# Kernel tuning notes

Measured on AMD Instinct MI355X. Metric: run time of the kernel, lower is better.

Reference implementation:

```python
import jax, jax.numpy as jnp
import numpy as np

F_DIM = 512
N_HEADS = 8
D_Q = 64
D_V = 64
EPS = 1e-6


def _xavier(key, shape):
    fan_in, fan_out = shape[0], shape[1]
    limit = float(np.sqrt(6.0 / (fan_in + fan_out)))
    return jax.random.uniform(key, shape, jnp.float32, -limit, limit)


def layer_norm(x, g, b):
    mu = jnp.mean(x, axis=-1, keepdims=True)
    var = jnp.mean(jnp.square(x - mu), axis=-1, keepdims=True)
    return (x - mu) * jax.lax.rsqrt(var + EPS) * g + b


def setup_inputs() -> dict:
    key = jax.random.key(0)
    ks = jax.random.split(key, 16)
    B, V, F = 4, 2048, F_DIM
    inp = {
        "texture_map1": jax.random.normal(ks[0], (B, V, F), jnp.float32),
        "texture_map2": jax.random.normal(ks[1], (B, V, F), jnp.float32),
        "ln1_g": jnp.ones((F,), jnp.float32), "ln1_b": jnp.zeros((F,), jnp.float32),
        "ln2_g": jnp.ones((F,), jnp.float32), "ln2_b": jnp.zeros((F,), jnp.float32),
        "Wq": _xavier(ks[2], (F, N_HEADS * D_Q)), "bq": jnp.zeros((N_HEADS * D_Q,), jnp.float32),
        "Wk": _xavier(ks[3], (F, N_HEADS * D_Q)), "bk": jnp.zeros((N_HEADS * D_Q,), jnp.float32),
        "Wv": _xavier(ks[4], (F, N_HEADS * D_V)), "bv": jnp.zeros((N_HEADS * D_V,), jnp.float32),
        "Wfc": _xavier(ks[5], (N_HEADS * D_V, F)), "bfc": jnp.zeros((F,), jnp.float32),
        "ff1_ln_g": jnp.ones((F,), jnp.float32), "ff1_ln_b": jnp.zeros((F,), jnp.float32),
        "ff1_W1": _xavier(ks[6], (F, F)), "ff1_b1": jnp.zeros((F,), jnp.float32),
        "ff1_W2": _xavier(ks[7], (F, F)), "ff1_b2": jnp.zeros((F,), jnp.float32),
        "ff2_ln_g": jnp.ones((F,), jnp.float32), "ff2_ln_b": jnp.zeros((F,), jnp.float32),
        "ff2_W1": _xavier(ks[8], (F, F)), "ff2_b1": jnp.zeros((F,), jnp.float32),
        "ff2_W2": _xavier(ks[9], (F, F)), "ff2_b2": jnp.zeros((F,), jnp.float32),
    }
    return inp


def _heads(x, d):
    B, V, _ = x.shape
    return x.reshape(B, V, N_HEADS, d).transpose(0, 2, 1, 3)  # [B,H,V,d]


def _ff_block(x, ln_g, ln_b, W1, b1, W2, b2):
    h = layer_norm(x, ln_g, ln_b)
    h = jax.nn.relu(h @ W1 + b1) @ W2 + b2
    return x + h


def reference(texture_map1, texture_map2, ln1_g, ln1_b, ln2_g, ln2_b,
              Wq, bq, Wk, bk, Wv, bv, Wfc, bfc,
              ff1_ln_g, ff1_ln_b, ff1_W1, ff1_b1, ff1_W2, ff1_b2,
              ff2_ln_g, ff2_ln_b, ff2_W1, ff2_b1, ff2_W2, ff2_b2):
    B, V, F = texture_map1.shape
    norm = D_Q ** 0.5
    t1n = layer_norm(texture_map1, ln1_g, ln1_b)
    t2n = layer_norm(texture_map2, ln2_g, ln2_b)
    q1 = _heads(t1n @ Wq + bq, D_Q)
    k1 = _heads(t1n @ Wk + bk, D_Q)
    v1 = _heads(t1n @ Wv + bv, D_V)
    q2 = _heads(t2n @ Wq + bq, D_Q)
    k2 = _heads(t2n @ Wk + bk, D_Q)
    v2 = _heads(t2n @ Wv + bv, D_V)
    # cross attention: 1 attends to 2, 2 attends to 1
    attn12 = jax.nn.softmax(jnp.einsum('bhqd,bhkd->bhqk', q1, k2) / norm, axis=-1)
    attn21 = jax.nn.softmax(jnp.einsum('bhqd,bhkd->bhqk', q2, k1) / norm, axis=-1)
    f12 = jnp.einsum('bhqk,bhkd->bhqd', attn12, v2).transpose(0, 2, 1, 3).reshape(B, V, -1)
    f21 = jnp.einsum('bhqk,bhkd->bhqd', attn21, v1).transpose(0, 2, 1, 3).reshape(B, V, -1)
    f12 = f12 @ Wfc + bfc
    f21 = f21 @ Wfc + bfc
    out1 = _ff_block(texture_map1 + f12, ff1_ln_g, ff1_ln_b, ff1_W1, ff1_b1, ff1_W2, ff1_b2)
    out2 = _ff_block(texture_map2 + f21, ff2_ln_g, ff2_ln_b, ff2_W1, ff2_b1, ff2_W2, ff2_b2)
    return (out1, out2)
```

## Files before the change

### kernel.cpp

```cpp
#include <hip/hip_runtime.h>
#include <stdint.h>

#define FD    512
#define SEQ   2048
#define NHALF 8192
#define NTOT  16384
#define QKVN  1536

typedef unsigned short u16;
typedef __attribute__((ext_vector_type(8))) short short8;
typedef __attribute__((ext_vector_type(4))) float f32x4;

__device__ __forceinline__ u16 f2bf(float f){
  union { float f; uint32_t i; } v; v.f = f;
  uint32_t r = v.i + 0x7FFFu + ((v.i >> 16) & 1u);
  return (u16)(r >> 16);
}

__device__ __forceinline__ void gload_lds16(const void* g, void* l){
  __builtin_amdgcn_global_load_lds((const __attribute__((address_space(1))) void*)g,
                                   (__attribute__((address_space(3))) void*)l, 16, 0, 0);
}

__device__ __forceinline__ f32x4 mfma16(short8 a, short8 b, f32x4 c){
  return __builtin_amdgcn_mfma_f32_16x16x32_bf16(a, b, c, 0, 0, 0);
}

__device__ __forceinline__ uint32_t cvtpk(float lo, float hi){
  uint32_t r; asm("v_cvt_pk_bf16_f32 %0, %1, %2" : "=v"(r) : "v"(lo), "v"(hi)); return r;
}

__device__ __forceinline__ float fexp2(float x){
  float r; asm("v_exp_f32 %0, %1" : "=v"(r) : "v"(x)); return r;
}

__global__ __launch_bounds__(256) void wconv_kernel(
    const float* __restrict__ w0, const float* __restrict__ w1,
    const float* __restrict__ w2, const float* __restrict__ w3,
    const float* __restrict__ w4, const float* __restrict__ w5,
    const float* __restrict__ w6, const float* __restrict__ w7,
    u16* __restrict__ out)
{
  int mat = blockIdx.x >> 6;
  const float* w = w0;
  switch (mat){ case 1: w=w1; break; case 2: w=w2; break; case 3: w=w3; break;
                case 4: w=w4; break; case 5: w=w5; break; case 6: w=w6; break;
                case 7: w=w7; break; default: break; }
  int tile = blockIdx.x & 63;
  int k0 = (tile >> 3) << 6, n0 = (tile & 7) << 6;

  __shared__ float lt[64][65];
  int tid = threadIdx.x;
  int tr = tid >> 4, tc = (tid & 15) << 2;
  #pragma unroll
  for (int p = 0; p < 4; p++){
    int k = p * 16 + tr;
    float4 v = *(const float4*)&w[(size_t)(k0 + k) * 512 + n0 + tc];
    lt[k][tc] = v.x; lt[k][tc + 1] = v.y; lt[k][tc + 2] = v.z; lt[k][tc + 3] = v.w;
  }
  __syncthreads();
  int n = tid >> 2, kc = (tid & 3) << 4;
  u16 buf[16];
  #pragma unroll
  for (int j = 0; j < 16; j++) buf[j] = f2bf(lt[kc + j][n]);
  u16* dst = out + ((size_t)mat << 18) + (size_t)(n0 + n) * 512 + k0 + kc;
  *(short8*)dst       = *(const short8*)(buf);
  *(short8*)(dst + 8) = *(const short8*)(buf + 8);
}

__global__ __launch_bounds__(256) void biascat_kernel(
    const float* __restrict__ bq, const float* __restrict__ bk,
    const float* __restrict__ bv, float* __restrict__ o)
{
  int i = blockIdx.x * 256 + threadIdx.x;
  if (i < 512) o[i] = bq[i];
  else if (i < 1024) o[i] = bk[i - 512];
  else o[i] = bv[i - 1024];
}

__global__ __launch_bounds__(256) void ln_kernel(
    const float* __restrict__ xa, const float* __restrict__ xb,
    const float* __restrict__ ga, const float* __restrict__ ba,
    const float* __restrict__ gb, const float* __restrict__ bb,
    u16* __restrict__ out)
{
  int row = blockIdx.x;
  const float* x; const float* g; const float* bi;
  if (row < NHALF){ x = xa + (size_t)row * FD; g = ga; bi = ba; }
  else            { x = xb + (size_t)(row - NHALF) * FD; g = gb; bi = bb; }
  int t = threadIdx.x;
  float2 v = ((const float2*)x)[t];
  __shared__ float red[8];
  float s = v.x + v.y;
  #pragma unroll
  for (int o = 32; o; o >>= 1) s += __shfl_xor(s, o, 64);
  if ((t & 63) == 0) red[t >> 6] = s;
  __syncthreads();
  float mu = (red[0] + red[1] + red[2] + red[3]) * (1.0f / 512.0f);
  float d0 = v.x - mu, d1 = v.y - mu;
  float q = d0 * d0 + d1 * d1;
  #pragma unroll
  for (int o = 32; o; o >>= 1) q += __shfl_xor(q, o, 64);
  if ((t & 63) == 0) red[4 + (t >> 6)] = q;
  __syncthreads();
  float var = (red[4] + red[5] + red[6] + red[7]) * (1.0f / 512.0f);
  float rs = rsqrtf(var + 1e-6f);
  out[(size_t)row * FD + 2 * t]     = f2bf(d0 * rs * g[2 * t]     + bi[2 * t]);
  out[(size_t)row * FD + 2 * t + 1] = f2bf(d1 * rs * g[2 * t + 1] + bi[2 * t + 1]);
}

__global__ __launch_bounds__(256) void vtr_kernel(
    const u16* __restrict__ qkv, u16* __restrict__ vt)
{
  int kc = blockIdx.x & 15;
  int s  = blockIdx.x >> 4;
  int dir = s >> 5, b = (s >> 3) & 3, h = s & 7;
  int t = threadIdx.x;
  int d = t & 63, kb = t >> 6;
  const u16* src = qkv + (size_t)(dir * NHALF + b * SEQ + kc * 128 + kb * 32) * QKVN
                       + 1024 + h * 64 + d;
  u16* dst = vt + (size_t)s * 131072 + (size_t)d * 2048 + kc * 128 + kb * 32;
  u16 buf[32];
  #pragma unroll
  for (int j = 0; j < 32; j++) buf[j] = src[(size_t)j * QKVN];
  #pragma unroll
  for (int j = 0; j < 4; j++)
    *(short8*)(dst + j * 8) = *(const short8*)(buf + j * 8);
}

template<bool RELU, bool OUT_BF16, bool HAS_RES>
__global__ __launch_bounds__(256) void gemm_bt(
    const u16* __restrict__ A,
    const u16* __restrict__ BtLo, const u16* __restrict__ BtHi,
    const float* __restrict__ biasLo, const float* __restrict__ biasHi,
    const float* __restrict__ resLo, const float* __restrict__ resHi,
    void* __restrict__ outp,
    int M, int N, int K, int halfM)
{
  __shared__ __align__(16) u16 lA[2][128 * 32];
  __shared__ __align__(16) u16 lB[2][128 * 32];
  int nTN = N >> 7;
  int bm = blockIdx.x / nTN, bn = blockIdx.x - bm * nTN;
  int rowBase = bm << 7, colBase = bn << 7;
  bool lo = rowBase < halfM;
  const u16* Bt = lo ? BtLo : BtHi;
  const float* bias = lo ? biasLo : biasHi;
  const float* res = lo ? resLo : resHi;
  int rowLocalBase = lo ? rowBase : rowBase - halfM;

  int tid = threadIdx.x, wv = tid >> 6, ln = tid & 63;

  f32x4 acc[4][4];
  #pragma unroll
  for (int m = 0; m < 4; m++)
    #pragma unroll
    for (int n = 0; n < 4; n++) acc[m][n] = (f32x4){0.f, 0.f, 0.f, 0.f};

  int off0 = tid * 16, off1 = 4096 + tid * 16;
  int r0 = off0 >> 6, c0 = (off0 & 63) >> 1;
  int r1 = off1 >> 6, c1 = (off1 & 63) >> 1;
  const u16* gA0 = A + (size_t)(rowBase + r0) * K + c0;
  const u16* gA1 = A + (size_t)(rowBase + r1) * K + c1;
  const u16* gB0 = Bt + (size_t)(colBase + r0) * K + c0;
  const u16* gB1 = Bt + (size_t)(colBase + r1) * K + c1;

  int arow = (wv >> 1) << 6, bcol = (wv & 1) << 6;

  #define STAGE(buf, kt) do { \
    gload_lds16(gA0 + (kt), (char*)lA[buf] + wv * 1024); \
    gload_lds16(gA1 + (kt), (char*)lA[buf] + 4096 + wv * 1024); \
    gload_lds16(gB0 + (kt), (char*)lB[buf] + wv * 1024); \
    gload_lds16(gB1 + (kt), (char*)lB[buf] + 4096 + wv * 1024); } while (0)

  STAGE(0, 0);
  __syncthreads();

  int nK = K >> 5;
  for (int i = 0; i < nK; i++){
    int cur = i & 1;
    if (i + 1 < nK) STAGE(cur ^ 1, (i + 1) << 5);
    short8 af[4], bfr[4];
    #pragma unroll
    for (int m = 0; m < 4; m++)
      af[m] = *(const short8*)&lA[cur][(arow + (m << 4) + (ln & 15)) * 32 + ((ln >> 4) << 3)];
    #pragma unroll
    for (int n = 0; n < 4; n++)
      bfr[n] = *(const short8*)&lB[cur][(bcol + (n << 4) + (ln & 15)) * 32 + ((ln >> 4) << 3)];
    #pragma unroll
    for (int m = 0; m < 4; m++)
      #pragma unroll
      for (int n = 0; n < 4; n++)
        acc[m][n] = mfma16(af[m], bfr[n], acc[m][n]);
    __syncthreads();
  }
  #undef STAGE

  #pragma unroll
  for (int n = 0; n < 4; n++){
    int col = colBase + bcol + (n << 4) + (ln & 15);
    float bv = bias[col];
    #pragma unroll
    for (int m = 0; m < 4; m++){
      int rowT = arow + (m << 4) + ((ln >> 4) << 2);
      #pragma unroll
      for (int r = 0; r < 4; r++){
        float v = acc[m][n][r] + bv;
        if (RELU) v = fmaxf(v, 0.f);
        if (HAS_RES) v += res[(size_t)(rowLocalBase + rowT + r) * N + col];
        if (OUT_BF16) ((u16*)outp)[(size_t)(rowBase + rowT + r) * N + col] = f2bf(v);
        else ((float*)outp)[(size_t)(rowBase + rowT + r) * N + col] = v;
      }
    }
  }
}

__global__ __launch_bounds__(512, 4) void attn_kernel(
    const u16* __restrict__ qkv, const u16* __restrict__ vt, u16* __restrict__ fb)
{
  int qt = blockIdx.x;
  int h  = blockIdx.y;
  int z  = blockIdx.z;
  int dir = z >> 2, b = z & 3;
  int qRow0  = dir * NHALF + b * SEQ + qt * 256;
  int kvRow0 = (dir ^ 1) * NHALF + b * SEQ;
  int colQ = h * 64;

  __shared__ __align__(16) u16 lK[2][64 * 64];
  __shared__ __align__(16) u16 lVt[2][64 * 64];
  __shared__ __align__(16) u16 lP[8][32 * 64];

  int tid = threadIdx.x, wv = tid >> 6, ln = tid & 63;
  int g = ln >> 4, lo = ln & 15;

  int srow = tid >> 3;
  int soff = ((tid & 7) ^ (srow & 7)) * 8;

  const float CEXP = 0.18033688f;

  int ca0 = (g * 8) ^ ((lo & 7) << 3);
  int ca1 = (32 + g * 8) ^ ((lo & 7) << 3);
  int lo64 = lo * 64;

  int pidx[4];
  #pragma unroll
  for (int n = 0; n < 4; n++)
    pidx[n] = lo64 + ((n * 16 + g * 4) ^ ((lo & 7) << 3));
  int pra = lo64 + ca0, prb = lo64 + ca1;

  const u16* qbase  = qkv + (size_t)qRow0 * QKVN + colQ;
  const u16* vtbase = vt + (size_t)((dir ^ 1) * 32 + b * 8 + h) * 131072;

  const u16* kp0 = qkv + (size_t)(kvRow0 + srow) * QKVN + 512 + colQ + soff;
  const u16* vp0 = vtbase + (size_t)srow * 2048 + soff;

  char* dK0 = (char*)lK[0] + wv * 1024;
  char* dV0 = (char*)lVt[0] + wv * 1024;
  const u16* lKf = &lK[0][0];
  const u16* lVf = &lVt[0][0];
  u16* lPw = &lP[wv][0];

  gload_lds16(qbase + (size_t)srow * QKVN + soff,         (char*)lK[0]  + wv * 1024);
  gload_lds16(qbase + (size_t)(64 + srow) * QKVN + soff,  (char*)lK[1]  + wv * 1024);
  gload_lds16(qbase + (size_t)(128 + srow) * QKVN + soff, (char*)lVt[0] + wv * 1024);
  gload_lds16(qbase + (size_t)(192 + srow) * QKVN + soff, (char*)lVt[1] + wv * 1024);
  __syncthreads();
  const u16* qh;
  switch (wv >> 1){ case 0: qh = lK[0]; break; case 1: qh = lK[1]; break;
                    case 2: qh = lVt[0]; break; default: qh = lVt[1]; break; }
  int qr0 = (wv & 1) * 32 + lo;
  short8 qf00 = *(const short8*)&qh[qr0 * 64 + ca0];
  short8 qf01 = *(const short8*)&qh[qr0 * 64 + ca1];
  short8 qf10 = *(const short8*)&qh[(qr0 + 16) * 64 + ca0];
  short8 qf11 = *(const short8*)&qh[(qr0 + 16) * 64 + ca1];
  __syncthreads();

  gload_lds16(kp0, dK0);
  gload_lds16(vp0, dV0);
  kp0 += (size_t)64 * QKVN; vp0 += 64;
  __syncthreads();

  f32x4 acc_o0[4], acc_o1[4];
  #pragma unroll
  for (int nd = 0; nd < 4; nd++){
    acc_o0[nd] = (f32x4){0.f, 0.f, 0.f, 0.f};
    acc_o1[nd] = (f32x4){0.f, 0.f, 0.f, 0.f};
  }
  f32x4 acc_l0 = (f32x4){0.f, 0.f, 0.f, 0.f};
  f32x4 acc_l1 = (f32x4){0.f, 0.f, 0.f, 0.f};
  float m_l0, m_l1;
  const f32x4 z4 = (f32x4){0.f, 0.f, 0.f, 0.f};

  short8 ones;
  #pragma unroll
  for (int j = 0; j < 8; j++) ones[j] = (short)0x3F80;

  int cb = 0;
  for (int t = 0; t < 32; t++){
    if (t < 31){
      int nb = cb ^ 8192;
      gload_lds16(kp0, dK0 + nb);
      gload_lds16(vp0, dV0 + nb);
      kp0 += (size_t)64 * QKVN; vp0 += 64;
    }
    const u16* lk = (const u16*)((const char*)lKf + cb);
    const u16* lv = (const u16*)((const char*)lVf + cb);

    f32x4 s0[4], s1[4];
    #pragma unroll
    for (int n = 0; n < 4; n++){
      short8 kfa = *(const short8*)&lk[lo64 + n * 1024 + ca0];
      short8 kfb = *(const short8*)&lk[lo64 + n * 1024 + ca1];
      s0[n] = mfma16(kfa, qf00, z4);
      s0[n] = mfma16(kfb, qf01, s0[n]);
      s1[n] = mfma16(kfa, qf10, z4);
      s1[n] = mfma16(kfb, qf11, s1[n]);
    }

    float m00, m01;
    {
      float t0 = fmaxf(fmaxf(s0[0][0], s0[0][1]), fmaxf(s0[0][2], s0[0][3]));
      float t1 = fmaxf(fmaxf(s0[1][0], s0[1][1]), fmaxf(s0[1][2], s0[1][3]));
      float t2 = fmaxf(fmaxf(s0[2][0], s0[2][1]), fmaxf(s0[2][2], s0[2][3]));
      float t3 = fmaxf(fmaxf(s0[3][0], s0[3][1]), fmaxf(s0[3][2], s0[3][3]));
      m00 = fmaxf(fmaxf(t0, t1), fmaxf(t2, t3));
      m00 = fmaxf(m00, __shfl_xor(m00, 16, 64));
      m00 = fmaxf(m00, __shfl_xor(m00, 32, 64));
      m00 *= CEXP;
    }
    {
      float t0 = fmaxf(fmaxf(s1[0][0], s1[0][1]), fmaxf(s1[0][2], s1[0][3]));
      float t1 = fmaxf(fmaxf(s1[1][0], s1[1][1]), fmaxf(s1[1][2], s1[1][3]));
      float t2 = fmaxf(fmaxf(s1[2][0], s1[2][1]), fmaxf(s1[2][2], s1[2][3]));
      float t3 = fmaxf(fmaxf(s1[3][0], s1[3][1]), fmaxf(s1[3][2], s1[3][3]));
      m01 = fmaxf(fmaxf(t0, t1), fmaxf(t2, t3));
      m01 = fmaxf(m01, __shfl_xor(m01, 16, 64));
      m01 = fmaxf(m01, __shfl_xor(m01, 32, 64));
      m01 *= CEXP;
    }

    if (t == 0){ m_l0 = m00; m_l1 = m01; }

    #pragma unroll
    for (int n = 0; n < 4; n++){
      float p0 = fexp2(fmaf(s0[n][0], CEXP, -m_l0));
      float p1 = fexp2(fmaf(s0[n][1], CEXP, -m_l0));
      float p2 = fexp2(fmaf(s0[n][2], CEXP, -m_l0));
      float p3 = fexp2(fmaf(s0[n][3], CEXP, -m_l0));
      uint2 pk0; pk0.x = cvtpk(p0, p1); pk0.y = cvtpk(p2, p3);
      *(uint2*)&lPw[pidx[n]] = pk0;
      float q0 = fexp2(fmaf(s1[n][0], CEXP, -m_l1));
      float q1 = fexp2(fmaf(s1[n][1], CEXP, -m_l1));
      float q2 = fexp2(fmaf(s1[n][2], CEXP, -m_l1));
      float q3 = fexp2(fmaf(s1[n][3], CEXP, -m_l1));
      uint2 pk1; pk1.x = cvtpk(q0, q1); pk1.y = cvtpk(q2, q3);
      *(uint2*)&lPw[pidx[n] + 1024] = pk1;
    }

    short8 pf00 = *(const short8*)&lPw[pra];
    short8 pf01 = *(const short8*)&lPw[prb];
    short8 pf10 = *(const short8*)&lPw[pra + 1024];
    short8 pf11 = *(const short8*)&lPw[prb + 1024];
    acc_l0 = mfma16(pf00, ones, acc_l0);
    acc_l0 = mfma16(pf01, ones, acc_l0);
    acc_l1 = mfma16(pf10, ones, acc_l1);
    acc_l1 = mfma16(pf11, ones, acc_l1);
    #pragma unroll
    for (int nd = 0; nd < 4; nd++){
      short8 vfa = *(const short8*)&lv[lo64 + nd * 1024 + ca0];
      short8 vfb = *(const short8*)&lv[lo64 + nd * 1024 + ca1];
      acc_o0[nd] = mfma16(pf00, vfa, acc_o0[nd]);
      acc_o0[nd] = mfma16(pf01, vfb, acc_o0[nd]);
      acc_o1[nd] = mfma16(pf10, vfa, acc_o1[nd]);
      acc_o1[nd] = mfma16(pf11, vfb, acc_o1[nd]);
    }

    bool ok = (m00 <= m_l0 + 8.f) && (m01 <= m_l1 + 8.f);
    if (!__all(ok)){
      float mn0 = fmaxf(m_l0, m00);
      float mn1 = fmaxf(m_l1, m01);
      float a00 = fexp2(m_l0 - mn0);
      float a01 = fexp2(m_l1 - mn1);
      m_l0 = mn0; m_l1 = mn1;
      #pragma unroll
      for (int r = 0; r < 4; r++){
        float ar0 = __shfl(a00, g * 4 + r, 64);
        float ar1 = __shfl(a01, g * 4 + r, 64);
        acc_l0[r] *= ar0;
        acc_l1[r] *= ar1;
        #pragma unroll
        for (int nd = 0; nd < 4; nd++){
          acc_o0[nd][r] *= ar0;
          acc_o1[nd][r] *= ar1;
        }
      }
    }

    cb ^= 8192;
    __syncthreads();
  }

  #pragma unroll
  for (int r = 0; r < 4; r++){
    float rl0 = 1.0f / acc_l0[r];
    float rl1 = 1.0f / acc_l1[r];
    #pragma unroll
    for (int nd = 0; nd < 4; nd++){
      int row0 = qRow0 + wv * 32 + g * 4 + r;
      int d    = colQ + (nd << 4) + lo;
      fb[(size_t)row0 * FD + d]        = f2bf(acc_o0[nd][r] * rl0);
      fb[(size_t)(row0 + 16) * FD + d] = f2bf(acc_o1[nd][r] * rl1);
    }
  }
}

extern "C" void kernel_launch(void* const* d_in, const int* in_sizes, int n_in,
                              void* d_out, int out_size, void* d_ws, size_t ws_size,
                              hipStream_t stream)
{
  const float* t1   = (const float*)d_in[0];
  const float* t2   = (const float*)d_in[1];
  const float* ln1g = (const float*)d_in[2];
  const float* ln1b = (const float*)d_in[3];
  const float* ln2g = (const float*)d_in[4];
  const float* ln2b = (const float*)d_in[5];
  const float* Wq   = (const float*)d_in[6];
  const float* bq   = (const float*)d_in[7];
  const float* Wk   = (const float*)d_in[8];
  const float* bk   = (const float*)d_in[9];
  const float* Wv   = (const float*)d_in[10];
  const float* bv   = (const float*)d_in[11];
  const float* Wfc  = (const float*)d_in[12];
  const float* bfc  = (const float*)d_in[13];
  const float* f1lg = (const float*)d_in[14];
  const float* f1lb = (const float*)d_in[15];
  const float* W11  = (const float*)d_in[16];
  const float* b11  = (const float*)d_in[17];
  const float* W12  = (const float*)d_in[18];
  const float* b12  = (const float*)d_in[19];
  const float* f2lg = (const float*)d_in[20];
  const float* f2lb = (const float*)d_in[21];
  const float* W21  = (const float*)d_in[22];
  const float* b21  = (const float*)d_in[23];
  const float* W22  = (const float*)d_in[24];
  const float* b22  = (const float*)d_in[25];

  char* ws = (char*)d_ws;
  const size_t MB = 1024 * 1024;
  u16* wt     = (u16*)ws;
  u16* tln    = (u16*)(ws + 4 * MB);
  u16* qkv    = (u16*)(ws + 20 * MB);
  u16* fb     = (u16*)(ws + 68 * MB);
  float* bqkv = (float*)(ws + 84 * MB);
  u16* vtb    = tln;
  u16* xln    = tln;
  u16* hb     = qkv;
  float* out  = (float*)d_out;

  wconv_kernel<<<512, 256, 0, stream>>>(Wq, Wk, Wv, Wfc, W11, W12, W21, W22, wt);
  biascat_kernel<<<6, 256, 0, stream>>>(bq, bk, bv, bqkv);
  ln_kernel<<<NTOT, 256, 0, stream>>>(t1, t2, ln1g, ln1b, ln2g, ln2b, tln);
  gemm_bt<false, true, false><<<1536, 256, 0, stream>>>(
      tln, wt, wt, bqkv, bqkv, nullptr, nullptr, qkv, NTOT, QKVN, FD, NTOT);
  vtr_kernel<<<1024, 256, 0, stream>>>(qkv, vtb);
  attn_kernel<<<dim3(8, 8, 8), 512, 0, stream>>>(qkv, vtb, fb);
  gemm_bt<false, false, true><<<512, 256, 0, stream>>>(
      fb, wt + 3 * 262144, wt + 3 * 262144, bfc, bfc, t1, t2, out, NTOT, FD, FD, NHALF);
  ln_kernel<<<NTOT, 256, 0, stream>>>(out, out + (size_t)NHALF * FD, f1lg, f1lb, f2lg, f2lb, xln);
  gemm_bt<true, true, false><<<512, 256, 0, stream>>>(
      xln, wt + 4 * 262144, wt + 6 * 262144, b11, b21, nullptr, nullptr, hb, NTOT, FD, FD, NHALF);
  gemm_bt<false, false, true><<<512, 256, 0, stream>>>(
      hb, wt + 5 * 262144, wt + 7 * 262144, b12, b22, out, out + (size_t)NHALF * FD, out, NTOT, FD, FD, NHALF);
}
```

Measured before the change: 247.6 us.

## Halve per-wave P staging buffer by processing key tile in two halves

The softmax probability tile is now written to LDS and consumed by the PV MFMAs in two 32-key halves instead of one 64-key pass. This halves the per-wave P scratch buffer, with a new swizzle for the smaller layout, and the launch bound is raised from 4 to 6 blocks per CU. The aim is to cut LDS footprint and register pressure so more blocks can be resident. In exchange the stages are serialized more finely and register limits tighten, which could cause spills.

```diff
diff --git a/kernel.cpp b/kernel.cpp
--- a/kernel.cpp
+++ b/kernel.cpp
@@ -214,7 +214,7 @@
   }
 }
 
-__global__ __launch_bounds__(512, 4) void attn_kernel(
+__global__ __launch_bounds__(512, 6) void attn_kernel(
     const u16* __restrict__ qkv, const u16* __restrict__ vt, u16* __restrict__ fb)
 {
   int qt = blockIdx.x;
@@ -227,7 +227,7 @@
 
   __shared__ __align__(16) u16 lK[2][64 * 64];
   __shared__ __align__(16) u16 lVt[2][64 * 64];
-  __shared__ __align__(16) u16 lP[8][32 * 64];
+  __shared__ __align__(16) u16 lP[8][32 * 32];
 
   int tid = threadIdx.x, wv = tid >> 6, ln = tid & 63;
   int g = ln >> 4, lo = ln & 15;
@@ -241,11 +241,10 @@
   int ca1 = (32 + g * 8) ^ ((lo & 7) << 3);
   int lo64 = lo * 64;
 
-  int pidx[4];
-  #pragma unroll
-  for (int n = 0; n < 4; n++)
-    pidx[n] = lo64 + ((n * 16 + g * 4) ^ ((lo & 7) << 3));
-  int pra = lo64 + ca0, prb = lo64 + ca1;
+  int sw = lo & 3;
+  int pwr0 = lo * 64 + (((g >> 1) ^ sw) << 4) + ((g & 1) << 3);
+  int pwr1 = lo * 64 + ((((g >> 1) + 2) ^ sw) << 4) + ((g & 1) << 3);
+  int prd  = lo * 64 + ((g ^ sw) << 4);
 
   const u16* qbase  = qkv + (size_t)qRow0 * QKVN + colQ;
   const u16* vtbase = vt + (size_t)((dir ^ 1) * 32 + b * 8 + h) * 131072;
@@ -257,7 +256,7 @@
   char* dV0 = (char*)lVt[0] + wv * 1024;
   const u16* lKf = &lK[0][0];
   const u16* lVf = &lVt[0][0];
-  u16* lPw = &lP[wv][0];
+  char* lPb = (char*)&lP[wv][0];
 
   gload_lds16(qbase + (size_t)srow * QKVN + soff,         (char*)lK[0]  + wv * 1024);
   gload_lds16(qbase + (size_t)(64 + srow) * QKVN + soff,  (char*)lK[1]  + wv * 1024);
@@ -340,38 +339,58 @@
 
     if (t == 0){ m_l0 = m00; m_l1 = m01; }
 
-    #pragma unroll
-    for (int n = 0; n < 4; n++){
-      float p0 = fexp2(fmaf(s0[n][0], CEXP, -m_l0));
-      float p1 = fexp2(fmaf(s0[n][1], CEXP, -m_l0));
-      float p2 = fexp2(fmaf(s0[n][2], CEXP, -m_l0));
-      float p3 = fexp2(fmaf(s0[n][3], CEXP, -m_l0));
-      uint2 pk0; pk0.x = cvtpk(p0, p1); pk0.y = cvtpk(p2, p3);
-      *(uint2*)&lPw[pidx[n]] = pk0;
-      float q0 = fexp2(fmaf(s1[n][0], CEXP, -m_l1));
-      float q1 = fexp2(fmaf(s1[n][1], CEXP, -m_l1));
-      float q2 = fexp2(fmaf(s1[n][2], CEXP, -m_l1));
-      float q3 = fexp2(fmaf(s1[n][3], CEXP, -m_l1));
-      uint2 pk1; pk1.x = cvtpk(q0, q1); pk1.y = cvtpk(q2, q3);
-      *(uint2*)&lPw[pidx[n] + 1024] = pk1;
-    }
-
-    short8 pf00 = *(const short8*)&lPw[pra];
-    short8 pf01 = *(const short8*)&lPw[prb];
-    short8 pf10 = *(const short8*)&lPw[pra + 1024];
-    short8 pf11 = *(const short8*)&lPw[prb + 1024];
-    acc_l0 = mfma16(pf00, ones, acc_l0);
-    acc_l0 = mfma16(pf01, ones, acc_l0);
-    acc_l1 = mfma16(pf10, ones, acc_l1);
-    acc_l1 = mfma16(pf11, ones, acc_l1);
-    #pragma unroll
-    for (int nd = 0; nd < 4; nd++){
-      short8 vfa = *(const short8*)&lv[lo64 + nd * 1024 + ca0];
-      short8 vfb = *(const short8*)&lv[lo64 + nd * 1024 + ca1];
-      acc_o0[nd] = mfma16(pf00, vfa, acc_o0[nd]);
-      acc_o0[nd] = mfma16(pf01, vfb, acc_o0[nd]);
-      acc_o1[nd] = mfma16(pf10, vfa, acc_o1[nd]);
-      acc_o1[nd] = mfma16(pf11, vfb, acc_o1[nd]);
+    {
+      uint2 w;
+      w.x = cvtpk(fexp2(fmaf(s0[0][0], CEXP, -m_l0)), fexp2(fmaf(s0[0][1], CEXP, -m_l0)));
+      w.y = cvtpk(fexp2(fmaf(s0[0][2], CEXP, -m_l0)), fexp2(fmaf(s0[0][3], CEXP, -m_l0)));
+      *(uint2*)(lPb + pwr0) = w;
+      w.x = cvtpk(fexp2(fmaf(s0[1][0], CEXP, -m_l0)), fexp2(fmaf(s0[1][1], CEXP, -m_l0)));
+      w.y = cvtpk(fexp2(fmaf(s0[1][2], CEXP, -m_l0)), fexp2(fmaf(s0[1][3], CEXP, -m_l0)));
+      *(uint2*)(lPb + pwr1) = w;
+      w.x = cvtpk(fexp2(fmaf(s1[0][0], CEXP, -m_l1)), fexp2(fmaf(s1[0][1], CEXP, -m_l1)));
+      w.y = cvtpk(fexp2(fmaf(s1[0][2], CEXP, -m_l1)), fexp2(fmaf(s1[0][3], CEXP, -m_l1)));
+      *(uint2*)(lPb + pwr0 + 1024) = w;
+      w.x = cvtpk(fexp2(fmaf(s1[1][0], CEXP, -m_l1)), fexp2(fmaf(s1[1][1], CEXP, -m_l1)));
+      w.y = cvtpk(fexp2(fmaf(s1[1][2], CEXP, -m_l1)), fexp2(fmaf(s1[1][3], CEXP, -m_l1)));
+      *(uint2*)(lPb + pwr1 + 1024) = w;
+
+      short8 pf0 = *(const short8*)(lPb + prd);
+      short8 pf1 = *(const short8*)(lPb + prd + 1024);
+      acc_l0 = mfma16(pf0, ones, acc_l0);
+      acc_l1 = mfma16(pf1, ones, acc_l1);
+      #pragma unroll
+      for (int nd = 0; nd < 4; nd++){
+        short8 vf = *(const short8*)&lv[lo64 + nd * 1024 + ca0];
+        acc_o0[nd] = mfma16(pf0, vf, acc_o0[nd]);
+        acc_o1[nd] = mfma16(pf1, vf, acc_o1[nd]);
+      }
+    }
+
+    {
+      uint2 w;
+      w.x = cvtpk(fexp2(fmaf(s0[2][0], CEXP, -m_l0)), fexp2(fmaf(s0[2][1], CEXP, -m_l0)));
+      w.y = cvtpk(fexp2(fmaf(s0[2][2], CEXP, -m_l0)), fexp2(fmaf(s0[2][3], CEXP, -m_l0)));
+      *(uint2*)(lPb + pwr0) = w;
+      w.x = cvtpk(fexp2(fmaf(s0[3][0], CEXP, -m_l0)), fexp2(fmaf(s0[3][1], CEXP, -m_l0)));
+      w.y = cvtpk(fexp2(fmaf(s0[3][2], CEXP, -m_l0)), fexp2(fmaf(s0[3][3], CEXP, -m_l0)));
+      *(uint2*)(lPb + pwr1) = w;
+      w.x = cvtpk(fexp2(fmaf(s1[2][0], CEXP, -m_l1)), fexp2(fmaf(s1[2][1], CEXP, -m_l1)));
+      w.y = cvtpk(fexp2(fmaf(s1[2][2], CEXP, -m_l1)), fexp2(fmaf(s1[2][3], CEXP, -m_l1)));
+      *(uint2*)(lPb + pwr0 + 1024) = w;
+      w.x = cvtpk(fexp2(fmaf(s1[3][0], CEXP, -m_l1)), fexp2(fmaf(s1[3][1], CEXP, -m_l1)));
+      w.y = cvtpk(fexp2(fmaf(s1[3][2], CEXP, -m_l1)), fexp2(fmaf(s1[3][3], CEXP, -m_l1)));
+      *(uint2*)(lPb + pwr1 + 1024) = w;
+
+      short8 pf0 = *(const short8*)(lPb + prd);
+      short8 pf1 = *(const short8*)(lPb + prd + 1024);
+      acc_l0 = mfma16(pf0, ones, acc_l0);
+      acc_l1 = mfma16(pf1, ones, acc_l1);
+      #pragma unroll
+      for (int nd = 0; nd < 4; nd++){
+        short8 vf = *(const short8*)&lv[lo64 + nd * 1024 + ca1];
+        acc_o0[nd] = mfma16(pf0, vf, acc_o0[nd]);
+        acc_o1[nd] = mfma16(pf1, vf, acc_o1[nd]);
+      }
     }
 
     bool ok = (m00 <= m_l0 + 8.f) && (m01 <= m_l1 + 8.f);
```

After: 559.1 us. +125.8%, slower.
